# Kernel tuning notes

Measured on AMD Instinct MI355X. Metric: run time of the kernel, lower is better.

Reference implementation:

```python
import jax, jax.numpy as jnp
import numpy as np
import math

NEG_INF = -1e38


def wkv_scan(w, u, k, v):
    """Numerically-stable RWKV WKV recurrence.
    w, u: [C] (w is already -exp(time_decay)); k, v: [B, T, C] -> y: [B, T, C]."""
    B, T, C = k.shape

    def step(carry, kv_t):
        a, b, pp = carry            # running num/den in log-max form, [B, C]
        kt, vt = kv_t               # [B, C]
        ww = u + kt
        q = jnp.maximum(pp, ww)
        e1 = jnp.exp(pp - q)
        e2 = jnp.exp(ww - q)
        y = (e1 * a + e2 * vt) / (e1 * b + e2)
        # state update with decay w
        ww2 = pp + w
        q2 = jnp.maximum(ww2, kt)
        e1b = jnp.exp(ww2 - q2)
        e2b = jnp.exp(kt - q2)
        return (e1b * a + e2b * vt, e1b * b + e2b, q2), y

    init = (jnp.zeros((B, C), k.dtype), jnp.zeros((B, C), k.dtype),
            jnp.full((B, C), NEG_INF, k.dtype))
    kT = jnp.swapaxes(k, 0, 1)      # [T, B, C]
    vT = jnp.swapaxes(v, 0, 1)
    _, ys = jax.lax.scan(step, init, (kT, vT))
    return jnp.swapaxes(ys, 0, 1)   # [B, T, C]


def setup_inputs() -> dict:
    key = jax.random.key(0)
    B, T, C = 16, 1024, 1024
    k1, k2, k3, k4 = jax.random.split(key, 4)
    x = jax.random.normal(k1, (B, T, C), dtype=jnp.float32)
    scale = 0.02
    Wk = jax.random.normal(k2, (C, C), dtype=jnp.float32) * scale
    Wr = jax.random.normal(k3, (C, C), dtype=jnp.float32) * scale
    Wo = jax.random.normal(k4, (C, C), dtype=jnp.float32) * scale
    # faithful parameter init from RWKVTimeMix.__init__
    h = np.arange(C, dtype=np.float64)
    decay_speed = -5.0 + 8.0 * (h / (C - 1)) ** (0.7 + 1.3 * 1)
    zigzag = (((np.arange(C) + 1) % 3) - 1) * 0.5
    time_first = np.ones(C) * math.log(0.3) + zigzag
    return {
        "x": x,
        "Wk": Wk,
        "Wr": Wr,
        "Wo": Wo,
        "time_decay": jnp.asarray(decay_speed, dtype=jnp.float32),
        "time_first": jnp.asarray(time_first, dtype=jnp.float32),
    }


def reference(x, Wk, Wr, Wo, time_decay, time_first):
    # k = key(x); r = receptance(x); NOTE: source uses receptance for v as well
    k = jnp.einsum('btc,hc->bth', x, Wk)
    r = jnp.einsum('btc,hc->bth', x, Wr)
    v = r  # faithful to source: v = self.receptance(input)
    w = -jnp.exp(time_decay)
    y = wkv_scan(w, time_first, k, v)
    out = jax.nn.sigmoid(r) * y
    return jnp.einsum('bth,ch->btc', out, Wo)
```

## Files before the change

### kernel.cpp

```cpp
#include <hip/hip_runtime.h>
#include <hip/hip_bf16.h>


typedef __attribute__((ext_vector_type(8))) short bf16x8;
typedef __attribute__((ext_vector_type(4))) float f32x4;
typedef unsigned short u16;

#define GK   1024
#define NKT  16
#define ROWB 2048l

#define NCH  16384
#define NC   16
#define CL   64

__device__ __forceinline__ void async_copy16(const void* g, void* l) {
    __builtin_amdgcn_global_load_lds(
        (const __attribute__((address_space(1))) void*)g,
        (__attribute__((address_space(3))) void*)l,
        16 , 0 , 0 );
}

__global__ __launch_bounds__(256) void cast_f32_bf16_kernel(
    const float* __restrict__ src, __hip_bfloat16* __restrict__ dst, int n)
{
    const int i = (blockIdx.x * 256 + threadIdx.x) * 4;
    if (i + 3 < n) {
        const f32x4 v = *(const f32x4*)(src + i);
        __hip_bfloat16 o[4];
        o[0] = __float2bfloat16(v[0]);
        o[1] = __float2bfloat16(v[1]);
        o[2] = __float2bfloat16(v[2]);
        o[3] = __float2bfloat16(v[3]);
        *(__attribute__((ext_vector_type(4))) short*)(dst + i) =
            *(__attribute__((ext_vector_type(4))) short*)o;
    }
}


#define PHASE(I0, STAGE_STMT) do {                                            \
    bf16x8 a00 = *(const bf16x8*)(As + arow + (I0) * 2048 + ck0);             \
    bf16x8 a01 = *(const bf16x8*)(As + arow + (I0) * 2048 + ck1);             \
    bf16x8 a10 = *(const bf16x8*)(As + arow + (I0 + 1) * 2048 + ck0);         \
    bf16x8 a11 = *(const bf16x8*)(As + arow + (I0 + 1) * 2048 + ck1);         \
    STAGE_STMT;                                                               \
    __builtin_amdgcn_s_barrier();                                             \
    asm volatile("s_waitcnt lgkmcnt(0)" ::: "memory");                        \
    __builtin_amdgcn_sched_barrier(0);                                        \
    __builtin_amdgcn_s_setprio(1);                                            \
    _Pragma("unroll")                                                         \
    for (int n = 0; n < 4; ++n) {                                             \
        acc[I0][n]     = __builtin_amdgcn_mfma_f32_16x16x32_bf16(             \
                             a00, bf[n][0], acc[I0][n], 0, 0, 0);             \
        acc[I0][n]     = __builtin_amdgcn_mfma_f32_16x16x32_bf16(             \
                             a01, bf[n][1], acc[I0][n], 0, 0, 0);             \
        acc[I0 + 1][n] = __builtin_amdgcn_mfma_f32_16x16x32_bf16(             \
                             a10, bf[n][0], acc[I0 + 1][n], 0, 0, 0);         \
        acc[I0 + 1][n] = __builtin_amdgcn_mfma_f32_16x16x32_bf16(             \
                             a11, bf[n][1], acc[I0 + 1][n], 0, 0, 0);         \
    }                                                                         \
    __builtin_amdgcn_s_setprio(0);                                            \
    __builtin_amdgcn_s_barrier();                                            \
} while (0)

template <typename OutT>
__global__ __launch_bounds__(512, 2) void gemm256_kernel(
    const __hip_bfloat16* __restrict__ A,
    const __hip_bfloat16* __restrict__ B0,
    const __hip_bfloat16* __restrict__ B1,
    OutT* __restrict__ C,
    int ldc, int nsplit, int ntn)
{
    __shared__ __align__(16) char lds[131072];

    const int tid = threadIdx.x;

    const int nwg = gridDim.x;
    const int cpx = nwg >> 3;
    const int wg  = blockIdx.x;
    const int swz = (wg & 7) * cpx + (wg >> 3);
    const int bm  = (swz / ntn) * 256;
    const int bn  = (swz % ntn) * 256;

    const __hip_bfloat16* Bsrc;
    int bnl;
    if (bn < nsplit) { Bsrc = B0; bnl = bn; }
    else             { Bsrc = B1; bnl = bn - nsplit; }

    const int lane = tid & 63;
    const int wave = tid >> 6;
    const int nl   = lane & 15;
    const int quad = lane >> 4;
    const int wm   = (wave >> 2) * 128;
    const int wn   = (wave & 3) * 64;

    const int r0 = tid >> 3;
    const int cs = ((tid & 7) ^ (r0 & 7)) << 4;
    const int od = tid * 16;
    const char* Ag = (const char*)A    + (size_t)(bm  + r0) * ROWB + cs;
    const char* Bg = (const char*)Bsrc + (size_t)(bnl + r0) * ROWB + cs;

    char* ldsA0 = lds;
    char* ldsB0 = lds + 32768;
    char* ldsA1 = lds + 65536;
    char* ldsB1 = lds + 98304;

    auto stageA = [&](int kt, int h, char* dstA) {
        const char* g = Ag + (size_t)h * 128 * ROWB + (size_t)kt * 128;
        async_copy16(g,             dstA + h * 16384 + od);
        async_copy16(g + 64 * ROWB, dstA + h * 16384 + od + 8192);
    };
    auto stageB = [&](int kt, int h, char* dstB) {
        const char* g = Bg + (size_t)h * 128 * ROWB + (size_t)kt * 128;
        async_copy16(g,             dstB + h * 16384 + od);
        async_copy16(g + 64 * ROWB, dstB + h * 16384 + od + 8192);
    };

    const int rw   = nl & 7;
    const int ck0  = (quad ^ rw) << 4;
    const int ck1  = ((4 + quad) ^ rw) << 4;
    const int arow = (wm + nl) * 128;
    const int brow = (wn + nl) * 128;

    f32x4 acc[8][4] = {};

    stageB(0, 0, ldsB0); stageB(0, 1, ldsB0);
    stageA(0, 0, ldsA0); stageA(0, 1, ldsA0);
    stageB(1, 0, ldsB1); stageB(1, 1, ldsB1);
    asm volatile("s_waitcnt vmcnt(4)" ::: "memory");
    __builtin_amdgcn_s_barrier();

#pragma unroll 2
    for (int t = 0; t < NKT; ++t) {
        char* As = (t & 1) ? ldsA1 : ldsA0;
        char* Bs = (t & 1) ? ldsB1 : ldsB0;
        char* Ao = (t & 1) ? ldsA0 : ldsA1;

        bf16x8 bf[4][2];
#pragma unroll
        for (int n = 0; n < 4; ++n) {
            bf[n][0] = *(const bf16x8*)(Bs + brow + n * 2048 + ck0);
            bf[n][1] = *(const bf16x8*)(Bs + brow + n * 2048 + ck1);
        }

        PHASE(0, if (t + 1 < NKT) stageA(t + 1, 0, Ao));
        PHASE(2, if (t + 1 < NKT) stageA(t + 1, 1, Ao));
        PHASE(4, if (t + 2 < NKT) stageB(t + 2, 0, Bs));
        PHASE(6, {
            if (t + 2 < NKT) {
                stageB(t + 2, 1, Bs);
                asm volatile("s_waitcnt vmcnt(4)" ::: "memory");
            } else {
                asm volatile("s_waitcnt vmcnt(0)" ::: "memory");
            }
        });
    }

#pragma unroll
    for (int i = 0; i < 8; ++i) {
#pragma unroll
        for (int n = 0; n < 4; ++n) {
            const int col = bn + wn + n * 16 + nl;
#pragma unroll
            for (int r = 0; r < 4; ++r) {
                const int m = bm + wm + i * 16 + quad * 4 + r;
                const float vv = acc[i][n][r];
                if constexpr (__is_same(OutT, float))
                    C[(size_t)m * ldc + col] = vv;
                else
                    C[(size_t)m * ldc + col] = __float2bfloat16(vv);
            }
        }
    }
}

#define L2E 1.4426950408889634f

struct Blk { u16 k[8]; u16 v[8]; };

__device__ __forceinline__ void load8(const u16* kp, const u16* vp,
                                      int t, int S, Blk& B) {
#pragma unroll
    for (int j = 0; j < 8; ++j) {
        B.k[j] = kp[(size_t)(t + j) * S];
        B.v[j] = vp[(size_t)(t + j) * S];
    }
}

__device__ __forceinline__ float bf2f(u16 r) {
    return __uint_as_float(((unsigned)r) << 16);
}

__device__ __forceinline__ void wkv_state_step(
    u16 kraw, u16 vraw, float w2, float& a, float& bb, float& pp2)
{
    const float kf = bf2f(kraw);
    const float vf = bf2f(vraw);
    const float k2 = kf * L2E;
    const float d   = pp2 + w2 - k2;
    const float m0  = fminf(d, 0.f);
    const float e1b = __builtin_amdgcn_exp2f(m0);
    const float e2b = __builtin_amdgcn_exp2f(m0 - d);
    a   = e1b * a  + e2b * vf;
    bb  = e1b * bb + e2b;
    pp2 = k2 + fmaxf(d, 0.f);
}

__device__ __forceinline__ void wkv_step(
    u16 kraw, u16 vraw, float u2, float w2,
    float& a, float& bb, float& pp2, __hip_bfloat16* op)
{
    const float kf = bf2f(kraw);
    const float vf = bf2f(vraw);
    const float k2 = kf * L2E;

    const float ww2 = u2 + k2;
    const float s   = __builtin_amdgcn_exp2f(fminf(pp2 - ww2, 60.f));
    const float num = s * a + vf;
    const float den = s * bb + 1.f;
    const float e   = __builtin_amdgcn_exp2f(-L2E * vf);
    const float res = num * __builtin_amdgcn_rcpf(den * (1.f + e));
    *op = __float2bfloat16(res);

    const float d   = pp2 + w2 - k2;
    const float m0  = fminf(d, 0.f);
    const float e1b = __builtin_amdgcn_exp2f(m0);
    const float e2b = __builtin_amdgcn_exp2f(m0 - d);
    a   = e1b * a  + e2b * vf;
    bb  = e1b * bb + e2b;
    pp2 = k2 + fmaxf(d, 0.f);
}

__global__ __launch_bounds__(256) void wkv_agg_kernel(
    const __hip_bfloat16* __restrict__ kr,
    const float* __restrict__ td,
    float* __restrict__ aggA, float* __restrict__ aggB,
    float* __restrict__ aggP, int T, int C)
{
    const int gid2  = blockIdx.x * 256 + threadIdx.x;
    const int ch    = gid2 & (NCH - 1);
    const int chunk = gid2 >> 14;
    const int b = ch >> 10;
    const int c = ch & (C - 1);
    const int S = 2 * C;

    const float w2 = -__expf(td[c]) * L2E;

    const u16* kp = (const u16*)(kr + (size_t)b * T * S + c)
                    + (size_t)(chunk * CL) * S;
    const u16* vp = kp + C;

    float a = 0.f, bb = 0.f, pp2 = -1.4427e38f;

    Blk A, Bq;
    load8(kp, vp, 0, S, A);
    for (int tb = 0; tb < CL; tb += 16) {
        load8(kp, vp, tb + 8, S, Bq);
#pragma unroll
        for (int j = 0; j < 8; ++j)
            wkv_state_step(A.k[j], A.v[j], w2, a, bb, pp2);
        if (tb + 16 < CL) load8(kp, vp, tb + 16, S, A);
#pragma unroll
        for (int j = 0; j < 8; ++j)
            wkv_state_step(Bq.k[j], Bq.v[j], w2, a, bb, pp2);
    }
    aggA[gid2] = a;
    aggB[gid2] = bb;
    aggP[gid2] = pp2;
}

__global__ __launch_bounds__(256) void wkv_out_kernel(
    const __hip_bfloat16* __restrict__ kr,
    const float* __restrict__ tf, const float* __restrict__ td,
    const float* __restrict__ aggA, const float* __restrict__ aggB,
    const float* __restrict__ aggP,
    __hip_bfloat16* __restrict__ sy, int T, int C)
{
    const int gid2  = blockIdx.x * 256 + threadIdx.x;
    const int ch    = gid2 & (NCH - 1);
    const int chunk = gid2 >> 14;
    const int b = ch >> 10;
    const int c = ch & (C - 1);
    const int S = 2 * C;

    const float u2 = tf[c] * L2E;
    const float w2 = -__expf(td[c]) * L2E;

    float a = 0.f, bb = 0.f, pp2 = -1.4427e38f;
    for (int j = 0; j < chunk; ++j) {
        const float p  = aggP[j * NCH + ch]
                         + (float)((chunk - 1 - j) * CL) * w2;
        const float Aj = aggA[j * NCH + ch];
        const float Bj = aggB[j * NCH + ch];
        const float q  = fmaxf(pp2, p);
        const float e1 = __builtin_amdgcn_exp2f(pp2 - q);
        const float e2 = __builtin_amdgcn_exp2f(p - q);
        a   = e1 * a  + e2 * Aj;
        bb  = e1 * bb + e2 * Bj;
        pp2 = q;
    }

    const int t0 = chunk * CL;
    const u16* kp = (const u16*)(kr + (size_t)b * T * S + c) + (size_t)t0 * S;
    const u16* vp = kp + C;
    __hip_bfloat16* op = sy + (size_t)b * T * C + (size_t)t0 * C + c;

    Blk A, Bq;
    load8(kp, vp, 0, S, A);
    for (int tb = 0; tb < CL; tb += 16) {
        load8(kp, vp, tb + 8, S, Bq);
#pragma unroll
        for (int j = 0; j < 8; ++j)
            wkv_step(A.k[j], A.v[j], u2, w2, a, bb, pp2,
                     op + (size_t)(tb + j) * C);
        if (tb + 16 < CL) load8(kp, vp, tb + 16, S, A);
#pragma unroll
        for (int j = 0; j < 8; ++j)
            wkv_step(Bq.k[j], Bq.v[j], u2, w2, a, bb, pp2,
                     op + (size_t)(tb + 8 + j) * C);
    }
}

extern "C" void kernel_launch(void* const* d_in, const int* in_sizes, int n_in,
                              void* d_out, int out_size, void* d_ws, size_t ws_size,
                              hipStream_t stream) {
    const float* x  = (const float*)d_in[0];
    const float* Wk = (const float*)d_in[1];
    const float* Wr = (const float*)d_in[2];
    const float* Wo = (const float*)d_in[3];
    const float* td = (const float*)d_in[4];
    const float* tf = (const float*)d_in[5];
    float* out = (float*)d_out;

    const int B = 16, T = 1024, C = 1024;
    const int M = B * T;
    const int MC = M * C;
    const int CC = C * C;

    __hip_bfloat16* xb  = (__hip_bfloat16*)d_ws;
    __hip_bfloat16* Wkb = xb + (size_t)MC;
    __hip_bfloat16* Wrb = Wkb + (size_t)CC;
    __hip_bfloat16* Wob = Wrb + (size_t)CC;
    __hip_bfloat16* sy  = xb;

    float* aggA = (float*)Wkb;
    float* aggB = aggA + (size_t)NCH * NC;
    float* aggP = (float*)Wrb;

    __hip_bfloat16* kr = (__hip_bfloat16*)d_out;

    cast_f32_bf16_kernel<<<MC / 1024, 256, 0, stream>>>(x,  xb,  MC);
    cast_f32_bf16_kernel<<<CC / 1024, 256, 0, stream>>>(Wk, Wkb, CC);
    cast_f32_bf16_kernel<<<CC / 1024, 256, 0, stream>>>(Wr, Wrb, CC);
    cast_f32_bf16_kernel<<<CC / 1024, 256, 0, stream>>>(Wo, Wob, CC);

    gemm256_kernel<__hip_bfloat16><<<dim3((M / 256) * (2 * C / 256)), 512, 0,
                                     stream>>>(xb, Wkb, Wrb, kr, 2 * C, C, 8);

    wkv_agg_kernel<<<dim3(NCH * NC / 256), 256, 0, stream>>>(
        kr, td, aggA, aggB, aggP, T, C);

    wkv_out_kernel<<<dim3(NCH * NC / 256), 256, 0, stream>>>(
        kr, tf, td, aggA, aggB, aggP, sy, T, C);

    gemm256_kernel<float><<<dim3((M / 256) * (C / 256)), 512, 0, stream>>>(
        sy, Wob, Wob, out, C, C, 4);
}
```

Measured before the change: 264.1 us.

## Software-pipeline LDS fragment loads across GEMM k-tile phases

Restructures the GEMM main loop so the A/B fragments for the next MFMA phase are read from LDS while the current phase's MFMAs run. It uses partial lgkmcnt waits instead of waiting for all loads, and reorders the phases by k-half rather than by row pair. The next tile's first fragments are prefetched at the end of each iteration. The aim is to hide LDS read latency behind matrix-core work, at the cost of more live fragment registers and more fragile wait-count accounting.

Result: slower. 354.3 us (+34.2%).

```diff
diff --git a/kernel.cpp b/kernel.cpp
--- a/kernel.cpp
+++ b/kernel.cpp
@@ -38,29 +38,13 @@
 }
 
 
-#define PHASE(I0, STAGE_STMT) do {                                            \
-    bf16x8 a00 = *(const bf16x8*)(As + arow + (I0) * 2048 + ck0);             \
-    bf16x8 a01 = *(const bf16x8*)(As + arow + (I0) * 2048 + ck1);             \
-    bf16x8 a10 = *(const bf16x8*)(As + arow + (I0 + 1) * 2048 + ck0);         \
-    bf16x8 a11 = *(const bf16x8*)(As + arow + (I0 + 1) * 2048 + ck1);         \
-    STAGE_STMT;                                                               \
-    __builtin_amdgcn_s_barrier();                                             \
-    asm volatile("s_waitcnt lgkmcnt(0)" ::: "memory");                        \
-    __builtin_amdgcn_sched_barrier(0);                                        \
-    __builtin_amdgcn_s_setprio(1);                                            \
+#define MFMA16(I0, AFR, BFR) do {                                             \
     _Pragma("unroll")                                                         \
-    for (int n = 0; n < 4; ++n) {                                             \
-        acc[I0][n]     = __builtin_amdgcn_mfma_f32_16x16x32_bf16(             \
-                             a00, bf[n][0], acc[I0][n], 0, 0, 0);             \
-        acc[I0][n]     = __builtin_amdgcn_mfma_f32_16x16x32_bf16(             \
-                             a01, bf[n][1], acc[I0][n], 0, 0, 0);             \
-        acc[I0 + 1][n] = __builtin_amdgcn_mfma_f32_16x16x32_bf16(             \
-                             a10, bf[n][0], acc[I0 + 1][n], 0, 0, 0);         \
-        acc[I0 + 1][n] = __builtin_amdgcn_mfma_f32_16x16x32_bf16(             \
-                             a11, bf[n][1], acc[I0 + 1][n], 0, 0, 0);         \
-    }                                                                         \
-    __builtin_amdgcn_s_setprio(0);                                            \
-    __builtin_amdgcn_s_barrier();                                            \
+    for (int i = 0; i < 4; ++i)                                               \
+        _Pragma("unroll")                                                     \
+        for (int n = 0; n < 4; ++n)                                           \
+            acc[(I0) + i][n] = __builtin_amdgcn_mfma_f32_16x16x32_bf16(       \
+                AFR[i], BFR[n], acc[(I0) + i][n], 0, 0, 0);                   \
 } while (0)
 
 template <typename OutT>
@@ -123,37 +107,95 @@
     const int brow = (wn + nl) * 128;
 
     f32x4 acc[8][4] = {};
+    bf16x8 aq[4], ar[4], bq0[4], bq1[4];
 
     stageB(0, 0, ldsB0); stageB(0, 1, ldsB0);
     stageA(0, 0, ldsA0); stageA(0, 1, ldsA0);
+    asm volatile("s_waitcnt vmcnt(0)" ::: "memory");
     stageB(1, 0, ldsB1); stageB(1, 1, ldsB1);
-    asm volatile("s_waitcnt vmcnt(4)" ::: "memory");
     __builtin_amdgcn_s_barrier();
+#pragma unroll
+    for (int i = 0; i < 4; ++i)
+        aq[i] = *(const bf16x8*)(ldsA0 + arow + i * 2048 + ck0);
+#pragma unroll
+    for (int n = 0; n < 4; ++n)
+        bq0[n] = *(const bf16x8*)(ldsB0 + brow + n * 2048 + ck0);
+    __builtin_amdgcn_sched_barrier(0);
 
 #pragma unroll 2
     for (int t = 0; t < NKT; ++t) {
         char* As = (t & 1) ? ldsA1 : ldsA0;
         char* Bs = (t & 1) ? ldsB1 : ldsB0;
-        char* Ao = (t & 1) ? ldsA0 : ldsA1;
-
-        bf16x8 bf[4][2];
-#pragma unroll
-        for (int n = 0; n < 4; ++n) {
-            bf[n][0] = *(const bf16x8*)(Bs + brow + n * 2048 + ck0);
-            bf[n][1] = *(const bf16x8*)(Bs + brow + n * 2048 + ck1);
+        char* An = (t & 1) ? ldsA0 : ldsA1;
+        char* Bn = (t & 1) ? ldsB0 : ldsB1;
+
+#pragma unroll
+        for (int i = 0; i < 4; ++i)
+            ar[i] = *(const bf16x8*)(As + arow + (4 + i) * 2048 + ck0);
+        __builtin_amdgcn_sched_barrier(0);
+        if (t + 1 < NKT) stageA(t + 1, 0, An);
+        __builtin_amdgcn_s_barrier();
+        asm volatile("s_waitcnt lgkmcnt(4)" ::: "memory");
+        __builtin_amdgcn_sched_barrier(0);
+        __builtin_amdgcn_s_setprio(1);
+        MFMA16(0, aq, bq0);
+        __builtin_amdgcn_s_setprio(0);
+        __builtin_amdgcn_s_barrier();
+
+#pragma unroll
+        for (int i = 0; i < 4; ++i)
+            aq[i] = *(const bf16x8*)(As + arow + i * 2048 + ck1);
+#pragma unroll
+        for (int n = 0; n < 4; ++n)
+            bq1[n] = *(const bf16x8*)(Bs + brow + n * 2048 + ck1);
+        __builtin_amdgcn_sched_barrier(0);
+        if (t + 1 < NKT) stageA(t + 1, 1, An);
+        __builtin_amdgcn_s_barrier();
+        asm volatile("s_waitcnt lgkmcnt(8)" ::: "memory");
+        __builtin_amdgcn_sched_barrier(0);
+        __builtin_amdgcn_s_setprio(1);
+        MFMA16(4, ar, bq0);
+        __builtin_amdgcn_s_setprio(0);
+        __builtin_amdgcn_s_barrier();
+
+#pragma unroll
+        for (int i = 0; i < 4; ++i)
+            ar[i] = *(const bf16x8*)(As + arow + (4 + i) * 2048 + ck1);
+        __builtin_amdgcn_sched_barrier(0);
+        __builtin_amdgcn_s_barrier();
+        asm volatile("s_waitcnt lgkmcnt(4)" ::: "memory");
+        __builtin_amdgcn_sched_barrier(0);
+        if (t + 2 < NKT) stageB(t + 2, 0, Bs);
+        __builtin_amdgcn_s_setprio(1);
+        MFMA16(0, aq, bq1);
+        __builtin_amdgcn_s_setprio(0);
+        __builtin_amdgcn_s_barrier();
+
+        if (t + 2 < NKT) {
+            stageB(t + 2, 1, Bs);
+            asm volatile("s_waitcnt vmcnt(4)" ::: "memory");
+        } else {
+            asm volatile("s_waitcnt vmcnt(0)" ::: "memory");
         }
-
-        PHASE(0, if (t + 1 < NKT) stageA(t + 1, 0, Ao));
-        PHASE(2, if (t + 1 < NKT) stageA(t + 1, 1, Ao));
-        PHASE(4, if (t + 2 < NKT) stageB(t + 2, 0, Bs));
-        PHASE(6, {
-            if (t + 2 < NKT) {
-                stageB(t + 2, 1, Bs);
-                asm volatile("s_waitcnt vmcnt(4)" ::: "memory");
-            } else {
-                asm volatile("s_waitcnt vmcnt(0)" ::: "memory");
-            }
-        });
+        if (t + 1 < NKT) {
+#pragma unroll
+            for (int i = 0; i < 4; ++i)
+                aq[i] = *(const bf16x8*)(An + arow + i * 2048 + ck0);
+#pragma unroll
+            for (int n = 0; n < 4; ++n)
+                bq0[n] = *(const bf16x8*)(Bn + brow + n * 2048 + ck0);
+        }
+        __builtin_amdgcn_sched_barrier(0);
+        __builtin_amdgcn_s_barrier();
+        if (t + 1 < NKT)
+            asm volatile("s_waitcnt lgkmcnt(8)" ::: "memory");
+        else
+            asm volatile("s_waitcnt lgkmcnt(0)" ::: "memory");
+        __builtin_amdgcn_sched_barrier(0);
+        __builtin_amdgcn_s_setprio(1);
+        MFMA16(4, ar, bq1);
+        __builtin_amdgcn_s_setprio(0);
+        __builtin_amdgcn_s_barrier();
     }
 
 #pragma unroll
```
